# Optimization experiments

Hardware: AMD Instinct MI355X
Metric: run time of the kernel (lower is better)

## Reference

```python
import jax, jax.numpy as jnp
import numpy as np

B, D, H = 512, 512, 512  # batch, input dim, hidden dim


def setup_inputs() -> dict:
    key = jax.random.key(0)
    ks = jax.random.split(key, 7)
    s = 1.0 / np.sqrt(D)
    return {
        "x": jax.random.normal(ks[0], (B, D), jnp.float32),
        "W1": jax.random.normal(ks[1], (D, H), jnp.float32) * s,
        "b1": jax.random.normal(ks[2], (H,), jnp.float32) * 0.01,
        "W2": jax.random.normal(ks[3], (H, H), jnp.float32) * s,
        "b2": jax.random.normal(ks[4], (H,), jnp.float32) * 0.01,
        "w3": jax.random.normal(ks[5], (H,), jnp.float32) * s,
        "b3": jax.random.normal(ks[6], (1,), jnp.float32) * 0.01,
    }


def _per_sample(xi, W1, b1, W2, b2, w3, b3):
    # Sequential layers applied to one sample; per-sample scalar loss.
    h = jax.nn.relu(xi @ W1 + b1)
    h = jax.nn.relu(h @ W2 + b2)
    return h @ w3 + b3[0]


def reference(x, W1, b1, W2, b2, w3, b3):
    # Forward pass (vectorized over the batch) -> per-sample losses [B].
    h = jax.nn.relu(x @ W1 + b1)
    h = jax.nn.relu(h @ W2 + b2)
    output = h @ w3 + b3[0]  # [B]

    # _autogram: per-sample Jacobian w.r.t. all layer parameters with a seed
    # of ones (grad = ones_like(output)); gramian accumulates J @ J.T per
    # parameter block. jax.vmap(jax.grad) == torch.vmap(vjp) with scalar seed 1.
    grad_fn = jax.grad(_per_sample, argnums=(1, 2, 3, 4, 5, 6))
    grads = jax.vmap(grad_fn, in_axes=(0, None, None, None, None, None, None))(
        x, W1, b1, W2, b2, w3, b3
    )  # pytree of per-sample grads, each leaf [B, *param_shape]

    bsz = x.shape[0]
    gramian = jnp.zeros((bsz, bsz), x.dtype)
    for g in grads:  # fixed small number of parameter tensors (matches per-layer loop)
        J = g.reshape(bsz, -1)  # [B, n_params_block]
        gramian = gramian + J @ J.T
    return output, gramian
```

## Files before the change

kernel.cpp:

```cpp
#include <hip/hip_runtime.h>
#include <hip/hip_bf16.h>


#define NN 512

typedef __attribute__((ext_vector_type(8))) short v8s;
typedef __attribute__((ext_vector_type(4))) float v4f;

static __device__ __forceinline__ unsigned short f2bf(float f) {
    union { float f; unsigned u; } v; v.f = f;
    unsigned r = v.u + 0x7FFF + ((v.u >> 16) & 1);
    return (unsigned short)(r >> 16);
}

__global__ __launch_bounds__(256) void prep(
    const float* __restrict__ x, const float* __restrict__ W2,
    const float* __restrict__ b3,
    unsigned short* __restrict__ xb, unsigned short* __restrict__ W2b,
    float* __restrict__ out) {
    const int idx = (blockIdx.x * 256 + threadIdx.x) * 4;
    float4 xv = *(const float4*)&x[idx];
    float4 wv = *(const float4*)&W2[idx];
    ushort4 xo, wo;
    xo.x = f2bf(xv.x); xo.y = f2bf(xv.y); xo.z = f2bf(xv.z); xo.w = f2bf(xv.w);
    wo.x = f2bf(wv.x); wo.y = f2bf(wv.y); wo.z = f2bf(wv.z); wo.w = f2bf(wv.w);
    *(ushort4*)&xb[idx] = xo;
    *(ushort4*)&W2b[idx] = wo;
    if (blockIdx.x == 0) {
        float b = b3[0];
        out[threadIdx.x] = b;
        out[threadIdx.x + 256] = b;
    }
}

__global__ __launch_bounds__(256) void fwd1(
    const float* __restrict__ X, const float* __restrict__ W1,
    const float* __restrict__ b1,
    float* __restrict__ H1, unsigned short* __restrict__ H1b) {
    __shared__ float As[32][34];
    __shared__ float Bs[32][34];
    const int t = threadIdx.x;
    const int tx = t & 15, ty = t >> 4;
    const int i0 = blockIdx.y * 32, j0 = blockIdx.x * 32;
    const int lr = t >> 3;
    const int lk = (t & 7) * 4;
    float acc[2][2] = {};
    for (int k0 = 0; k0 < NN; k0 += 32) {
        float4 av = *(const float4*)&X [(i0 + lr) * NN + k0 + lk];
        float4 bv = *(const float4*)&W1[(k0 + lr) * NN + j0 + lk];
        __syncthreads();
        As[lk + 0][lr] = av.x; As[lk + 1][lr] = av.y;
        As[lk + 2][lr] = av.z; As[lk + 3][lr] = av.w;
        Bs[lr][lk + 0] = bv.x; Bs[lr][lk + 1] = bv.y;
        Bs[lr][lk + 2] = bv.z; Bs[lr][lk + 3] = bv.w;
        __syncthreads();
        #pragma unroll
        for (int k = 0; k < 32; ++k) {
            float2 a2 = *(const float2*)&As[k][2 * ty];
            float2 b2 = *(const float2*)&Bs[k][2 * tx];
            acc[0][0] += a2.x * b2.x; acc[0][1] += a2.x * b2.y;
            acc[1][0] += a2.y * b2.x; acc[1][1] += a2.y * b2.y;
        }
    }
    #pragma unroll
    for (int ii = 0; ii < 2; ++ii) {
        const int i = i0 + 2 * ty + ii;
        #pragma unroll
        for (int jj = 0; jj < 2; ++jj) {
            const int j = j0 + 2 * tx + jj;
            float v = acc[ii][jj] + b1[j];
            float h = v > 0.f ? v : 0.f;
            H1[i * NN + j] = h;
            H1b[i * NN + j] = f2bf(h);
        }
    }
}

__global__ __launch_bounds__(256) void fwd2(
    const float* __restrict__ H1, const float* __restrict__ W2,
    const float* __restrict__ b2, const float* __restrict__ w3,
    unsigned short* __restrict__ H2b, unsigned short* __restrict__ G2b,
    float* __restrict__ out) {
    __shared__ float As[32][34];
    __shared__ float Bs[32][34];
    __shared__ float rsum[32];
    const int t = threadIdx.x;
    const int tx = t & 15, ty = t >> 4;
    const int i0 = blockIdx.y * 32, j0 = blockIdx.x * 32;
    const int lr = t >> 3;
    const int lk = (t & 7) * 4;
    if (t < 32) rsum[t] = 0.f;
    float acc[2][2] = {};
    for (int k0 = 0; k0 < NN; k0 += 32) {
        float4 av = *(const float4*)&H1[(i0 + lr) * NN + k0 + lk];
        float4 bv = *(const float4*)&W2[(k0 + lr) * NN + j0 + lk];
        __syncthreads();
        As[lk + 0][lr] = av.x; As[lk + 1][lr] = av.y;
        As[lk + 2][lr] = av.z; As[lk + 3][lr] = av.w;
        Bs[lr][lk + 0] = bv.x; Bs[lr][lk + 1] = bv.y;
        Bs[lr][lk + 2] = bv.z; Bs[lr][lk + 3] = bv.w;
        __syncthreads();
        #pragma unroll
        for (int k = 0; k < 32; ++k) {
            float2 a2 = *(const float2*)&As[k][2 * ty];
            float2 b2v = *(const float2*)&Bs[k][2 * tx];
            acc[0][0] += a2.x * b2v.x; acc[0][1] += a2.x * b2v.y;
            acc[1][0] += a2.y * b2v.x; acc[1][1] += a2.y * b2v.y;
        }
    }
    float w3v[2], bias[2];
    #pragma unroll
    for (int jj = 0; jj < 2; ++jj) {
        w3v[jj]  = w3[j0 + 2 * tx + jj];
        bias[jj] = b2[j0 + 2 * tx + jj];
    }
    float rowc[2] = {0.f, 0.f};
    #pragma unroll
    for (int ii = 0; ii < 2; ++ii) {
        const int i = i0 + 2 * ty + ii;
        #pragma unroll
        for (int jj = 0; jj < 2; ++jj) {
            const int j = j0 + 2 * tx + jj;
            float z = acc[ii][jj] + bias[jj];
            float h = z > 0.f ? z : 0.f;
            H2b[i * NN + j] = f2bf(h);
            G2b[i * NN + j] = (z > 0.f) ? f2bf(w3v[jj]) : (unsigned short)0;
            rowc[ii] += h * w3v[jj];
        }
    }
    #pragma unroll
    for (int ii = 0; ii < 2; ++ii)
        atomicAdd(&rsum[2 * ty + ii], rowc[ii]);
    __syncthreads();
    if (t < 32) atomicAdd(&out[i0 + t], rsum[t]);
}

__global__ __launch_bounds__(256) void g1k(
    const unsigned short* __restrict__ G2b, const unsigned short* __restrict__ W2b,
    const float* __restrict__ H1, unsigned short* __restrict__ G1b) {
    const int t = threadIdx.x;
    const int wave = t >> 6, lane = t & 63;
    const int r = lane & 15, quad = lane >> 4;
    const int i0 = blockIdx.y * 32 + 16 * (wave >> 1);
    const int c0 = blockIdx.x * 32 + 16 * (wave & 1);
    const unsigned short* arow = G2b + (i0 + r) * NN + quad * 8;
    const unsigned short* brow = W2b + (c0 + r) * NN + quad * 8;
    v4f acc = {0.f, 0.f, 0.f, 0.f};
    #pragma unroll
    for (int k0 = 0; k0 < NN; k0 += 32) {
        v8s a = *(const v8s*)(arow + k0);
        v8s b = *(const v8s*)(brow + k0);
        acc = __builtin_amdgcn_mfma_f32_16x16x32_bf16(a, b, acc, 0, 0, 0);
    }
    #pragma unroll
    for (int rr = 0; rr < 4; ++rr) {
        const int i = i0 + quad * 4 + rr;
        const int c = c0 + r;
        float v = (H1[i * NN + c] > 0.f) ? acc[rr] : 0.f;
        G1b[i * NN + c] = f2bf(v);
    }
}

__global__ __launch_bounds__(256) void gramk(
    const unsigned short* __restrict__ Xb, const unsigned short* __restrict__ H1b,
    const unsigned short* __restrict__ G1b, const unsigned short* __restrict__ H2b,
    const unsigned short* __restrict__ G2b, float* __restrict__ gram) {
    const int t = threadIdx.x;
    const int wave = t >> 6, lane = t & 63;
    const int r = lane & 15, quad = lane >> 4;
    const int i0 = blockIdx.y * 32 + 16 * (wave >> 1);
    const int j0 = blockIdx.x * 32 + 16 * (wave & 1);
    const int ao = (i0 + r) * NN + quad * 8;
    const int bo = (j0 + r) * NN + quad * 8;
    v4f a0 = {0.f,0.f,0.f,0.f}, a1 = a0, a2 = a0, a3 = a0, a4 = a0;
    #pragma unroll
    for (int k0 = 0; k0 < NN; k0 += 32) {
        v8s xa = *(const v8s*)(Xb  + ao + k0), xb2 = *(const v8s*)(Xb  + bo + k0);
        v8s ha = *(const v8s*)(H1b + ao + k0), hb  = *(const v8s*)(H1b + bo + k0);
        v8s ga = *(const v8s*)(G1b + ao + k0), gb  = *(const v8s*)(G1b + bo + k0);
        v8s ua = *(const v8s*)(H2b + ao + k0), ub  = *(const v8s*)(H2b + bo + k0);
        v8s va = *(const v8s*)(G2b + ao + k0), vb  = *(const v8s*)(G2b + bo + k0);
        a0 = __builtin_amdgcn_mfma_f32_16x16x32_bf16(xa, xb2, a0, 0, 0, 0);
        a1 = __builtin_amdgcn_mfma_f32_16x16x32_bf16(ha, hb,  a1, 0, 0, 0);
        a2 = __builtin_amdgcn_mfma_f32_16x16x32_bf16(ga, gb,  a2, 0, 0, 0);
        a3 = __builtin_amdgcn_mfma_f32_16x16x32_bf16(ua, ub,  a3, 0, 0, 0);
        a4 = __builtin_amdgcn_mfma_f32_16x16x32_bf16(va, vb,  a4, 0, 0, 0);
    }
    #pragma unroll
    for (int rr = 0; rr < 4; ++rr) {
        const int i = i0 + quad * 4 + rr;
        const int j = j0 + r;
        float g = 1.f + a3[rr] + a4[rr] * (1.f + a1[rr]) + a2[rr] * (1.f + a0[rr]);
        gram[i * NN + j] = g;
    }
}

extern "C" void kernel_launch(void* const* d_in, const int* in_sizes, int n_in,
                              void* d_out, int out_size, void* d_ws, size_t ws_size,
                              hipStream_t stream) {
    const float* x  = (const float*)d_in[0];
    const float* W1 = (const float*)d_in[1];
    const float* b1 = (const float*)d_in[2];
    const float* W2 = (const float*)d_in[3];
    const float* b2 = (const float*)d_in[4];
    const float* w3 = (const float*)d_in[5];
    const float* b3 = (const float*)d_in[6];

    float* out  = (float*)d_out;
    float* gram = out + NN;

    float* H1           = (float*)d_ws;
    unsigned short* xb  = (unsigned short*)(H1 + NN * NN);
    unsigned short* W2b = xb  + NN * NN;
    unsigned short* H1b = W2b + NN * NN;
    unsigned short* H2b = H1b + NN * NN;
    unsigned short* G2b = H2b + NN * NN;
    unsigned short* G1b = G2b + NN * NN;

    dim3 blk(256);
    prep<<<dim3(256), blk, 0, stream>>>(x, W2, b3, xb, W2b, out);
    fwd1<<<dim3(16, 16), blk, 0, stream>>>(x, W1, b1, H1, H1b);
    fwd2<<<dim3(16, 16), blk, 0, stream>>>(H1, W2, b2, w3, H2b, G2b, out);
    g1k <<<dim3(16, 16), blk, 0, stream>>>(G2b, W2b, H1, G1b);
    gramk<<<dim3(16, 16), blk, 0, stream>>>(xb, H1b, G1b, H2b, G2b, gram);
}
```

Baseline: 125.9 us.

## Run forward GEMMs on bf16 MFMA with hi/lo split-precision emulation

Replaces the scalar fp32 shared-memory forward GEMMs with MFMA bf16 kernels that emulate fp32 accuracy through a three-product hi/lo split (hh + lh + hl). The prep kernel now also transposes W1 and W2 and splits x and the weights into hi/lo bf16 parts. The row-sum for the output uses wave shuffles instead of shared-memory atomics, and g1k reads the bf16 H1 for its ReLU mask, so the fp32 H1 buffer is no longer needed. It trades extra prep work, memory traffic and three MFMAs per step for moving the forward passes off the slow scalar FMA path.

Result: faster. 114.7 us (-8.9%).

```diff
diff --git a/kernel.cpp b/kernel.cpp
--- a/kernel.cpp
+++ b/kernel.cpp
@@ -1,5 +1,4 @@
 #include <hip/hip_runtime.h>
-#include <hip/hip_bf16.h>
 
 
 #define NN 512
@@ -12,132 +11,139 @@
     unsigned r = v.u + 0x7FFF + ((v.u >> 16) & 1);
     return (unsigned short)(r >> 16);
 }
+static __device__ __forceinline__ float bf2f(unsigned short h) {
+    union { unsigned u; float f; } v; v.u = ((unsigned)h) << 16;
+    return v.f;
+}
 
 __global__ __launch_bounds__(256) void prep(
-    const float* __restrict__ x, const float* __restrict__ W2,
-    const float* __restrict__ b3,
-    unsigned short* __restrict__ xb, unsigned short* __restrict__ W2b,
-    float* __restrict__ out) {
-    const int idx = (blockIdx.x * 256 + threadIdx.x) * 4;
-    float4 xv = *(const float4*)&x[idx];
-    float4 wv = *(const float4*)&W2[idx];
-    ushort4 xo, wo;
-    xo.x = f2bf(xv.x); xo.y = f2bf(xv.y); xo.z = f2bf(xv.z); xo.w = f2bf(xv.w);
-    wo.x = f2bf(wv.x); wo.y = f2bf(wv.y); wo.z = f2bf(wv.z); wo.w = f2bf(wv.w);
-    *(ushort4*)&xb[idx] = xo;
-    *(ushort4*)&W2b[idx] = wo;
-    if (blockIdx.x == 0) {
-        float b = b3[0];
-        out[threadIdx.x] = b;
-        out[threadIdx.x + 256] = b;
-    }
+    const float* __restrict__ x, const float* __restrict__ W1,
+    const float* __restrict__ W2, const float* __restrict__ b3,
+    unsigned short* __restrict__ xhi, unsigned short* __restrict__ xlo,
+    unsigned short* __restrict__ W1th, unsigned short* __restrict__ W1tl,
+    unsigned short* __restrict__ W2th, unsigned short* __restrict__ W2tl,
+    unsigned short* __restrict__ W2b, float* __restrict__ out) {
+    __shared__ float T[32][33];
+    const int t = threadIdx.x;
+    const int lr = t >> 3, lc = (t & 7) * 4;
+    const int r0 = blockIdx.y * 32, c0 = blockIdx.x * 32;
+    const int z = blockIdx.z;
+    if (z == 2) {
+        float4 v = *(const float4*)&x[(r0 + lr) * NN + c0 + lc];
+        ushort4 hi, lo;
+        hi.x = f2bf(v.x); lo.x = f2bf(v.x - bf2f(hi.x));
+        hi.y = f2bf(v.y); lo.y = f2bf(v.y - bf2f(hi.y));
+        hi.z = f2bf(v.z); lo.z = f2bf(v.z - bf2f(hi.z));
+        hi.w = f2bf(v.w); lo.w = f2bf(v.w - bf2f(hi.w));
+        *(ushort4*)&xhi[(r0 + lr) * NN + c0 + lc] = hi;
+        *(ushort4*)&xlo[(r0 + lr) * NN + c0 + lc] = lo;
+        if (blockIdx.x == 0 && t < 32) out[r0 + t] = b3[0];
+        return;
+    }
+    const float* src = (z == 1) ? W2 : W1;
+    float4 v = *(const float4*)&src[(r0 + lr) * NN + c0 + lc];
+    if (z == 1) {
+        ushort4 h;
+        h.x = f2bf(v.x); h.y = f2bf(v.y); h.z = f2bf(v.z); h.w = f2bf(v.w);
+        *(ushort4*)&W2b[(r0 + lr) * NN + c0 + lc] = h;
+    }
+    T[lr][lc + 0] = v.x; T[lr][lc + 1] = v.y;
+    T[lr][lc + 2] = v.z; T[lr][lc + 3] = v.w;
+    __syncthreads();
+    unsigned short* dh = (z == 1) ? W2th : W1th;
+    unsigned short* dl = (z == 1) ? W2tl : W1tl;
+    float a0 = T[lc + 0][lr], a1 = T[lc + 1][lr];
+    float a2 = T[lc + 2][lr], a3 = T[lc + 3][lr];
+    ushort4 hi, lo;
+    hi.x = f2bf(a0); lo.x = f2bf(a0 - bf2f(hi.x));
+    hi.y = f2bf(a1); lo.y = f2bf(a1 - bf2f(hi.y));
+    hi.z = f2bf(a2); lo.z = f2bf(a2 - bf2f(hi.z));
+    hi.w = f2bf(a3); lo.w = f2bf(a3 - bf2f(hi.w));
+    *(ushort4*)&dh[(c0 + lr) * NN + r0 + lc] = hi;
+    *(ushort4*)&dl[(c0 + lr) * NN + r0 + lc] = lo;
 }
 
 __global__ __launch_bounds__(256) void fwd1(
-    const float* __restrict__ X, const float* __restrict__ W1,
-    const float* __restrict__ b1,
-    float* __restrict__ H1, unsigned short* __restrict__ H1b) {
-    __shared__ float As[32][34];
-    __shared__ float Bs[32][34];
-    const int t = threadIdx.x;
-    const int tx = t & 15, ty = t >> 4;
-    const int i0 = blockIdx.y * 32, j0 = blockIdx.x * 32;
-    const int lr = t >> 3;
-    const int lk = (t & 7) * 4;
-    float acc[2][2] = {};
-    for (int k0 = 0; k0 < NN; k0 += 32) {
-        float4 av = *(const float4*)&X [(i0 + lr) * NN + k0 + lk];
-        float4 bv = *(const float4*)&W1[(k0 + lr) * NN + j0 + lk];
-        __syncthreads();
-        As[lk + 0][lr] = av.x; As[lk + 1][lr] = av.y;
-        As[lk + 2][lr] = av.z; As[lk + 3][lr] = av.w;
-        Bs[lr][lk + 0] = bv.x; Bs[lr][lk + 1] = bv.y;
-        Bs[lr][lk + 2] = bv.z; Bs[lr][lk + 3] = bv.w;
-        __syncthreads();
-        #pragma unroll
-        for (int k = 0; k < 32; ++k) {
-            float2 a2 = *(const float2*)&As[k][2 * ty];
-            float2 b2 = *(const float2*)&Bs[k][2 * tx];
-            acc[0][0] += a2.x * b2.x; acc[0][1] += a2.x * b2.y;
-            acc[1][0] += a2.y * b2.x; acc[1][1] += a2.y * b2.y;
-        }
-    }
-    #pragma unroll
-    for (int ii = 0; ii < 2; ++ii) {
-        const int i = i0 + 2 * ty + ii;
-        #pragma unroll
-        for (int jj = 0; jj < 2; ++jj) {
-            const int j = j0 + 2 * tx + jj;
-            float v = acc[ii][jj] + b1[j];
-            float h = v > 0.f ? v : 0.f;
-            H1[i * NN + j] = h;
-            H1b[i * NN + j] = f2bf(h);
-        }
+    const unsigned short* __restrict__ Ahi, const unsigned short* __restrict__ Alo,
+    const unsigned short* __restrict__ Bhi, const unsigned short* __restrict__ Blo,
+    const float* __restrict__ bias,
+    unsigned short* __restrict__ Chi, unsigned short* __restrict__ Clo) {
+    const int t = threadIdx.x;
+    const int wave = t >> 6, lane = t & 63;
+    const int r = lane & 15, quad = lane >> 4;
+    const int i0 = blockIdx.y * 32 + 16 * (wave >> 1);
+    const int j0 = blockIdx.x * 32 + 16 * (wave & 1);
+    const int ao = (i0 + r) * NN + quad * 8;
+    const int bo = (j0 + r) * NN + quad * 8;
+    v4f hh = {0.f, 0.f, 0.f, 0.f}, lh = hh, hl = hh;
+    #pragma unroll
+    for (int k0 = 0; k0 < NN; k0 += 32) {
+        v8s ah = *(const v8s*)(Ahi + ao + k0);
+        v8s al = *(const v8s*)(Alo + ao + k0);
+        v8s bh = *(const v8s*)(Bhi + bo + k0);
+        v8s bl = *(const v8s*)(Blo + bo + k0);
+        hh = __builtin_amdgcn_mfma_f32_16x16x32_bf16(ah, bh, hh, 0, 0, 0);
+        lh = __builtin_amdgcn_mfma_f32_16x16x32_bf16(al, bh, lh, 0, 0, 0);
+        hl = __builtin_amdgcn_mfma_f32_16x16x32_bf16(ah, bl, hl, 0, 0, 0);
+    }
+    const float bj = bias[j0 + r];
+    #pragma unroll
+    for (int rr = 0; rr < 4; ++rr) {
+        const int i = i0 + quad * 4 + rr, j = j0 + r;
+        float zv = (hh[rr] + lh[rr]) + hl[rr] + bj;
+        float h = zv > 0.f ? zv : 0.f;
+        unsigned short hi = f2bf(h);
+        Chi[i * NN + j] = hi;
+        Clo[i * NN + j] = f2bf(h - bf2f(hi));
     }
 }
 
 __global__ __launch_bounds__(256) void fwd2(
-    const float* __restrict__ H1, const float* __restrict__ W2,
+    const unsigned short* __restrict__ Ahi, const unsigned short* __restrict__ Alo,
+    const unsigned short* __restrict__ Bhi, const unsigned short* __restrict__ Blo,
     const float* __restrict__ b2, const float* __restrict__ w3,
     unsigned short* __restrict__ H2b, unsigned short* __restrict__ G2b,
     float* __restrict__ out) {
-    __shared__ float As[32][34];
-    __shared__ float Bs[32][34];
-    __shared__ float rsum[32];
-    const int t = threadIdx.x;
-    const int tx = t & 15, ty = t >> 4;
-    const int i0 = blockIdx.y * 32, j0 = blockIdx.x * 32;
-    const int lr = t >> 3;
-    const int lk = (t & 7) * 4;
-    if (t < 32) rsum[t] = 0.f;
-    float acc[2][2] = {};
-    for (int k0 = 0; k0 < NN; k0 += 32) {
-        float4 av = *(const float4*)&H1[(i0 + lr) * NN + k0 + lk];
-        float4 bv = *(const float4*)&W2[(k0 + lr) * NN + j0 + lk];
-        __syncthreads();
-        As[lk + 0][lr] = av.x; As[lk + 1][lr] = av.y;
-        As[lk + 2][lr] = av.z; As[lk + 3][lr] = av.w;
-        Bs[lr][lk + 0] = bv.x; Bs[lr][lk + 1] = bv.y;
-        Bs[lr][lk + 2] = bv.z; Bs[lr][lk + 3] = bv.w;
-        __syncthreads();
-        #pragma unroll
-        for (int k = 0; k < 32; ++k) {
-            float2 a2 = *(const float2*)&As[k][2 * ty];
-            float2 b2v = *(const float2*)&Bs[k][2 * tx];
-            acc[0][0] += a2.x * b2v.x; acc[0][1] += a2.x * b2v.y;
-            acc[1][0] += a2.y * b2v.x; acc[1][1] += a2.y * b2v.y;
-        }
-    }
-    float w3v[2], bias[2];
-    #pragma unroll
-    for (int jj = 0; jj < 2; ++jj) {
-        w3v[jj]  = w3[j0 + 2 * tx + jj];
-        bias[jj] = b2[j0 + 2 * tx + jj];
-    }
-    float rowc[2] = {0.f, 0.f};
-    #pragma unroll
-    for (int ii = 0; ii < 2; ++ii) {
-        const int i = i0 + 2 * ty + ii;
-        #pragma unroll
-        for (int jj = 0; jj < 2; ++jj) {
-            const int j = j0 + 2 * tx + jj;
-            float z = acc[ii][jj] + bias[jj];
-            float h = z > 0.f ? z : 0.f;
-            H2b[i * NN + j] = f2bf(h);
-            G2b[i * NN + j] = (z > 0.f) ? f2bf(w3v[jj]) : (unsigned short)0;
-            rowc[ii] += h * w3v[jj];
-        }
-    }
-    #pragma unroll
-    for (int ii = 0; ii < 2; ++ii)
-        atomicAdd(&rsum[2 * ty + ii], rowc[ii]);
-    __syncthreads();
-    if (t < 32) atomicAdd(&out[i0 + t], rsum[t]);
+    const int t = threadIdx.x;
+    const int wave = t >> 6, lane = t & 63;
+    const int r = lane & 15, quad = lane >> 4;
+    const int i0 = blockIdx.y * 32 + 16 * (wave >> 1);
+    const int j0 = blockIdx.x * 32 + 16 * (wave & 1);
+    const int ao = (i0 + r) * NN + quad * 8;
+    const int bo = (j0 + r) * NN + quad * 8;
+    v4f hh = {0.f, 0.f, 0.f, 0.f}, lh = hh, hl = hh;
+    #pragma unroll
+    for (int k0 = 0; k0 < NN; k0 += 32) {
+        v8s ah = *(const v8s*)(Ahi + ao + k0);
+        v8s al = *(const v8s*)(Alo + ao + k0);
+        v8s bh = *(const v8s*)(Bhi + bo + k0);
+        v8s bl = *(const v8s*)(Blo + bo + k0);
+        hh = __builtin_amdgcn_mfma_f32_16x16x32_bf16(ah, bh, hh, 0, 0, 0);
+        lh = __builtin_amdgcn_mfma_f32_16x16x32_bf16(al, bh, lh, 0, 0, 0);
+        hl = __builtin_amdgcn_mfma_f32_16x16x32_bf16(ah, bl, hl, 0, 0, 0);
+    }
+    const float bj = b2[j0 + r];
+    const float wj = w3[j0 + r];
+    const unsigned short wjb = f2bf(wj);
+    #pragma unroll
+    for (int rr = 0; rr < 4; ++rr) {
+        const int i = i0 + quad * 4 + rr, j = j0 + r;
+        float zv = (hh[rr] + lh[rr]) + hl[rr] + bj;
+        float h = zv > 0.f ? zv : 0.f;
+        H2b[i * NN + j] = f2bf(h);
+        G2b[i * NN + j] = (zv > 0.f) ? wjb : (unsigned short)0;
+        float p = h * wj;
+        p += __shfl_xor(p, 1, 64);
+        p += __shfl_xor(p, 2, 64);
+        p += __shfl_xor(p, 4, 64);
+        p += __shfl_xor(p, 8, 64);
+        if (r == 0) atomicAdd(&out[i], p);
+    }
 }
 
 __global__ __launch_bounds__(256) void g1k(
     const unsigned short* __restrict__ G2b, const unsigned short* __restrict__ W2b,
-    const float* __restrict__ H1, unsigned short* __restrict__ G1b) {
+    const unsigned short* __restrict__ H1b, unsigned short* __restrict__ G1b) {
     const int t = threadIdx.x;
     const int wave = t >> 6, lane = t & 63;
     const int r = lane & 15, quad = lane >> 4;
@@ -156,7 +162,7 @@
     for (int rr = 0; rr < 4; ++rr) {
         const int i = i0 + quad * 4 + rr;
         const int c = c0 + r;
-        float v = (H1[i * NN + c] > 0.f) ? acc[rr] : 0.f;
+        float v = (H1b[i * NN + c] != 0) ? acc[rr] : 0.f;
         G1b[i * NN + c] = f2bf(v);
     }
 }
@@ -209,18 +215,26 @@
     float* out  = (float*)d_out;
     float* gram = out + NN;
 
-    float* H1           = (float*)d_ws;
-    unsigned short* xb  = (unsigned short*)(H1 + NN * NN);
-    unsigned short* W2b = xb  + NN * NN;
-    unsigned short* H1b = W2b + NN * NN;
-    unsigned short* H2b = H1b + NN * NN;
-    unsigned short* G2b = H2b + NN * NN;
-    unsigned short* G1b = G2b + NN * NN;
+    unsigned short* p    = (unsigned short*)d_ws;
+    unsigned short* xhi  = p;  p += NN * NN;
+    unsigned short* xlo  = p;  p += NN * NN;
+    unsigned short* W1th = p;  p += NN * NN;
+    unsigned short* W1tl = p;  p += NN * NN;
+    unsigned short* W2th = p;  p += NN * NN;
+    unsigned short* W2tl = p;  p += NN * NN;
+    unsigned short* W2b  = p;  p += NN * NN;
+    unsigned short* H1b  = p;  p += NN * NN;
+    unsigned short* H1lo = p;  p += NN * NN;
+    unsigned short* H2b  = p;  p += NN * NN;
+    unsigned short* G2b  = p;  p += NN * NN;
+    unsigned short* G1b  = p;  p += NN * NN;
 
     dim3 blk(256);
-    prep<<<dim3(256), blk, 0, stream>>>(x, W2, b3, xb, W2b, out);
-    fwd1<<<dim3(16, 16), blk, 0, stream>>>(x, W1, b1, H1, H1b);
-    fwd2<<<dim3(16, 16), blk, 0, stream>>>(H1, W2, b2, w3, H2b, G2b, out);
-    g1k <<<dim3(16, 16), blk, 0, stream>>>(G2b, W2b, H1, G1b);
-    gramk<<<dim3(16, 16), blk, 0, stream>>>(xb, H1b, G1b, H2b, G2b, gram);
-}
+    prep <<<dim3(16, 16, 3), blk, 0, stream>>>(x, W1, W2, b3, xhi, xlo,
+                                               W1th, W1tl, W2th, W2tl, W2b, out);
+    fwd1 <<<dim3(16, 16), blk, 0, stream>>>(xhi, xlo, W1th, W1tl, b1, H1b, H1lo);
+    fwd2 <<<dim3(16, 16), blk, 0, stream>>>(H1b, H1lo, W2th, W2tl, b2, w3,
+                                            H2b, G2b, out);
+    g1k  <<<dim3(16, 16), blk, 0, stream>>>(G2b, W2b, H1b, G1b);
+    gramk<<<dim3(16, 16), blk, 0, stream>>>(xhi, H1b, G1b, H2b, G2b, gram);
+}
```
